# Performance work log

Hardware: AMD Instinct MI355X
Metric: run time of the kernel (lower is better)

## Reference

```python
import jax, jax.numpy as jnp
import numpy as np

DECAY = 0.99
EPS = 1e-05
B, T, DIM, N_EMBED = 64, 1024, 256, 1024


def setup_inputs() -> dict:
    key = jax.random.key(0)
    k1, k2 = jax.random.split(key, 2)
    input_ = jax.random.normal(k1, (B, T, DIM), dtype=jnp.float32)
    embed = jax.random.normal(k2, (DIM, N_EMBED), dtype=jnp.float32)  # buffer 'embed'
    cluster_size = jnp.zeros((N_EMBED,), dtype=jnp.float32)           # buffer 'cluster_size'
    embed_avg = embed.copy()                                          # buffer 'embed_avg'
    return {"input_": input_, "embed": embed, "cluster_size": cluster_size, "embed_avg": embed_avg}


def reference(input_, embed, cluster_size, embed_avg):
    n_embed = embed.shape[1]
    flatten = input_.reshape(-1, embed.shape[0])  # [N, dim]
    dist = (jnp.sum(flatten * flatten, axis=-1, keepdims=True)
            - 2.0 * flatten @ embed
            + jnp.sum(embed * embed, axis=0, keepdims=True))
    embed_ind = jnp.argmin(dist, axis=1)  # (-dist).max(1) == argmin(dist)
    quantize = jnp.take(embed.T, embed_ind, axis=0).reshape(input_.shape)

    # training-mode EMA codebook update (buffers are detached in torch)
    # embed_onehot_sum = onehot.sum(0); embed_sum = flatten.T @ onehot
    # implemented via segment_sum (same math, no NxK one-hot materialized)
    ones = jnp.ones((flatten.shape[0],), dtype=flatten.dtype)
    embed_onehot_sum = jax.ops.segment_sum(ones, embed_ind, num_segments=n_embed)
    embed_sum = jax.ops.segment_sum(flatten, embed_ind, num_segments=n_embed).T  # [dim, n_embed]

    new_cluster_size = cluster_size * DECAY + (1.0 - DECAY) * embed_onehot_sum
    # NOTE: original code applies .mul_(decay) TWICE to embed_avg -> decay**2 (faithful)
    new_embed_avg = embed_avg * (DECAY * DECAY) + (1.0 - DECAY) * embed_sum
    n = jnp.sum(new_cluster_size)
    cs = (new_cluster_size + EPS) / (n + n_embed * EPS) * n
    new_embed = new_embed_avg / cs[None, :]

    diff = jnp.mean((jax.lax.stop_gradient(quantize) - input_) ** 2)
    quantize_st = input_ + jax.lax.stop_gradient(quantize - input_)
    return quantize_st, diff, embed_ind, new_cluster_size, new_embed_avg, new_embed
```

## Files before the change

kernel.cpp:

```cpp
#include <hip/hip_runtime.h>
#include <float.h>

#define DECAY 0.99f
#define EPS 1e-5f
#define NROWS 65536
#define DIM 256
#define NEMB 1024
#define CH 64
#define MAXSUB 2048

#define GLOBAL_AS __attribute__((address_space(1)))
#define LOCAL_AS  __attribute__((address_space(3)))

typedef _Float16 f16;
typedef _Float16 half8 __attribute__((ext_vector_type(8)));
typedef float f32x4 __attribute__((ext_vector_type(4)));

__global__ __launch_bounds__(256) void k_enorm(const float* __restrict__ embed,
                                               float* __restrict__ enorm2,
                                               int* __restrict__ counts) {
    int kk = threadIdx.x & 63;
    int dg = threadIdx.x >> 6;
    int k  = blockIdx.x * 64 + kk;
    float s = 0.f;
    for (int d = dg; d < DIM; d += 4) {
        float v = embed[(size_t)d * NEMB + k];
        s = fmaf(v, v, s);
    }
    __shared__ float red[4][64];
    red[dg][kk] = s;
    __syncthreads();
    if (dg == 0) enorm2[k] = red[0][kk] + red[1][kk] + red[2][kk] + red[3][kk];
    int gt = blockIdx.x * 256 + threadIdx.x;
    if (gt < NEMB) counts[gt] = 0;
}

__global__ __launch_bounds__(256) void k_prep(const float* __restrict__ embed,
                                              float* __restrict__ embedT,
                                              f16* __restrict__ ehlT) {
    __shared__ float tile[32][33];
    int c0 = blockIdx.x * 32, d0 = blockIdx.y * 32;
    int tx = threadIdx.x, ty = threadIdx.y;
#pragma unroll
    for (int i = 0; i < 4; i++)
        tile[ty + 8 * i][tx] = embed[(size_t)(d0 + ty + 8 * i) * NEMB + c0 + tx];
    __syncthreads();
#pragma unroll
    for (int i = 0; i < 4; i++) {
        int c = c0 + ty + 8 * i;
        int d = d0 + tx;
        float v = tile[tx][ty + 8 * i];
        embedT[(size_t)c * DIM + d] = v;
        f16 h = (f16)v;
        ehlT[(size_t)c * 512 + d]       = h;
        ehlT[(size_t)c * 512 + 256 + d] = (f16)(v - (float)h);
    }
}

#define LDS_A  0
#define LDS_B0 131072
#define LDS_B1 147456
#define LDS_SZ 163840

__global__ __launch_bounds__(512, 2) void k_argmin_mfma(const float* __restrict__ input,
                                                        const f16* __restrict__ ehlT,
                                                        const float* __restrict__ enorm2,
                                                        int* __restrict__ ind,
                                                        float* __restrict__ out_ind) {
    __shared__ char lds[LDS_SZ];
    const int tid  = threadIdx.x;
    const int lane = tid & 63;
    const int w    = tid >> 6;
    const int wr   = w >> 2;
    const int wc   = w & 3;
    const int rb   = blockIdx.x * 128;
    const int l15  = lane & 15;
    const int lkh  = lane >> 4;
    const int swa  = (l15 & 7) << 4;
    const int swb  = ((l15 >> 1) & 3) << 4;
    const int slot_log   = (lane & 3) ^ ((lane >> 3) & 3);
    const int gl_laneoff = (lane >> 2) * 512 + slot_log * 8;

#pragma unroll
    for (int i = 0; i < 2; i++) {
        int chunkid = w * 2 + i;
        const f16* src = ehlT + (size_t)chunkid * 8192 + gl_laneoff;
        __builtin_amdgcn_global_load_lds((const GLOBAL_AS unsigned*)src,
            (LOCAL_AS unsigned*)(lds + LDS_B0 + chunkid * 1024), 16, 0, 0);
    }

#pragma unroll
    for (int it8 = 0; it8 < 4; it8++) {
        int task = tid + 512 * it8;
        int row = task >> 4, ch = task & 15;
        const float4* g = (const float4*)(input + (size_t)(rb + row) * DIM + ch * 16);
        float fv[16];
        *(float4*)(fv + 0)  = g[0];
        *(float4*)(fv + 4)  = g[1];
        *(float4*)(fv + 8)  = g[2];
        *(float4*)(fv + 12) = g[3];
        half8 hh[2], llv[2];
#pragma unroll
        for (int u = 0; u < 2; u++)
#pragma unroll
            for (int e = 0; e < 8; e++) {
                float x = fv[u * 8 + e];
                f16 h = (f16)x;
                hh[u][e]  = h;
                llv[u][e] = (f16)(x - (float)h);
            }
        int rbase = row * 1024;
        int sw = (row & 7) << 4;
        *(half8*)(lds + LDS_A + rbase + (((ch * 2    ) * 16) ^ sw)) = hh[0];
        *(half8*)(lds + LDS_A + rbase + (((ch * 2 + 1) * 16) ^ sw)) = hh[1];
        *(half8*)(lds + LDS_A + rbase + (((32 + ch * 2) * 16) ^ sw)) = llv[0];
        *(half8*)(lds + LDS_A + rbase + (((33 + ch * 2) * 16) ^ sw)) = llv[1];
    }
    __syncthreads();

    float bv[16];
    int   bi[16];
#pragma unroll
    for (int q = 0; q < 16; q++) { bv[q] = FLT_MAX; bi[q] = 0x7fffffff; }

    int p = 0;
    for (int ct = 0; ct < 4; ct++) {
        const int cb = ct * 256;
        f32x4 acc[4][4];
#pragma unroll
        for (int fr = 0; fr < 4; fr++)
#pragma unroll
            for (int fc = 0; fc < 4; fc++) acc[fr][fc] = (f32x4){0.f, 0.f, 0.f, 0.f};

        for (int kt = 0; kt < 24; kt++) {
            const int it = ct * 24 + kt;
            if (it < 95) {
                int itn = it + 1;
                int ct2 = itn / 24;
                int kt2 = itn - ct2 * 24;
                int seg2 = kt2 >> 3, kq2 = kt2 & 7;
                int koff2 = ((seg2 == 2) ? 256 : 0) + kq2 * 32;
                const f16* base = ehlT + (size_t)ct2 * 131072 + koff2 + gl_laneoff;
                char* dstb = lds + (p ? LDS_B0 : LDS_B1);
#pragma unroll
                for (int i = 0; i < 2; i++) {
                    int chunkid = w * 2 + i;
                    __builtin_amdgcn_global_load_lds(
                        (const GLOBAL_AS unsigned*)(base + (size_t)chunkid * 8192),
                        (LOCAL_AS unsigned*)(dstb + chunkid * 1024), 16, 0, 0);
                }
            }
            const int seg = kt >> 3, kq = kt & 7;
            const int jslot = ((seg == 1) ? 32 : 0) + kq * 4 + lkh;
            const char* Bb = lds + (p ? LDS_B1 : LDS_B0);
            half8 af[4], bf[4];
#pragma unroll
            for (int f = 0; f < 4; f++) {
                int row = wr * 64 + f * 16 + l15;
                af[f] = *(const half8*)(lds + LDS_A + row * 1024 + ((jslot * 16) ^ swa));
            }
#pragma unroll
            for (int f = 0; f < 4; f++) {
                int col = wc * 64 + f * 16 + l15;
                bf[f] = *(const half8*)(Bb + col * 64 + ((lkh * 16) ^ swb));
            }
#pragma unroll
            for (int fr = 0; fr < 4; fr++)
#pragma unroll
                for (int fc = 0; fc < 4; fc++)
                    acc[fr][fc] = __builtin_amdgcn_mfma_f32_16x16x32_f16(
                        af[fr], bf[fc], acc[fr][fc], 0, 0, 0);
            if (kt == 23) {
#pragma unroll
                for (int fc = 0; fc < 4; fc++) {
                    int col = cb + wc * 64 + fc * 16 + l15;
                    float e2 = enorm2[col];
#pragma unroll
                    for (int fr = 0; fr < 4; fr++)
#pragma unroll
                        for (int r = 0; r < 4; r++) {
                            float s = fmaf(-2.f, acc[fr][fc][r], e2);
                            int q = fr * 4 + r;
                            if (s < bv[q]) { bv[q] = s; bi[q] = col; }
                        }
                }
            }
            __syncthreads();
            p ^= 1;
        }
    }

#pragma unroll
    for (int q = 0; q < 16; q++) {
        float v = bv[q]; int i = bi[q];
#pragma unroll
        for (int m = 1; m <= 8; m <<= 1) {
            float ov = __shfl_xor(v, m, 64);
            int   oi = __shfl_xor(i, m, 64);
            if (ov < v || (ov == v && oi < i)) { v = ov; i = oi; }
        }
        bv[q] = v; bi[q] = i;
    }
    float* PV = (float*)(lds + LDS_B0);
    int*   PI = (int*)(lds + LDS_B0 + 2048);
    if (l15 == 0) {
#pragma unroll
        for (int fr = 0; fr < 4; fr++)
#pragma unroll
            for (int r = 0; r < 4; r++) {
                int rrow = wr * 64 + fr * 16 + lkh * 4 + r;
                PV[rrow * 4 + wc] = bv[fr * 4 + r];
                PI[rrow * 4 + wc] = bi[fr * 4 + r];
            }
    }
    __syncthreads();
    if (tid < 128) {
        float best = FLT_MAX; int bidx = 0x7fffffff;
#pragma unroll
        for (int t = 0; t < 4; t++) {
            float v = PV[tid * 4 + t];
            int   i = PI[tid * 4 + t];
            if (v < best || (v == best && i < bidx)) { best = v; bidx = i; }
        }
        ind[rb + tid] = bidx;
        out_ind[rb + tid] = (float)bidx;
    }
}

__global__ __launch_bounds__(256) void k_quant(const float* __restrict__ input,
                                               const float* __restrict__ embedT,
                                               const int* __restrict__ ind,
                                               float* __restrict__ out_q,
                                               float* __restrict__ partials) {
    const int tid = threadIdx.x;
    const unsigned gid = blockIdx.x * 256 + tid;
    float s = 0.f;
#pragma unroll
    for (int j = 0; j < 8; j++) {
        size_t i4 = (size_t)gid + (size_t)j * 524288u;
        int row = (int)(i4 >> 6);
        int d4  = (int)(i4 & 63);
        float4 iv = *reinterpret_cast<const float4*>(input + i4 * 4);
        int k = ind[row];
        float4 qv = *reinterpret_cast<const float4*>(embedT + (size_t)k * DIM + d4 * 4);
        float dx = qv.x - iv.x, dy = qv.y - iv.y, dz = qv.z - iv.z, dw = qv.w - iv.w;
        float4 ov;
        ov.x = iv.x + dx; ov.y = iv.y + dy; ov.z = iv.z + dz; ov.w = iv.w + dw;
        *reinterpret_cast<float4*>(out_q + i4 * 4) = ov;
        s += dx * dx + dy * dy + dz * dz + dw * dw;
    }
    __shared__ float red[256];
    red[tid] = s;
    __syncthreads();
    for (int off = 128; off > 0; off >>= 1) {
        if (tid < off) red[tid] += red[tid + off];
        __syncthreads();
    }
    if (tid == 0) partials[blockIdx.x] = red[0];
}

__global__ __launch_bounds__(256) void k_diff(const float* __restrict__ partials,
                                              float* __restrict__ out_diff) {
    __shared__ float red[256];
    int tid = threadIdx.x;
    float s = 0.f;
    for (int j = 0; j < 8; j++) s += partials[tid * 8 + j];
    red[tid] = s;
    __syncthreads();
    for (int off = 128; off > 0; off >>= 1) {
        if (tid < off) red[tid] += red[tid + off];
        __syncthreads();
    }
    if (tid == 0) out_diff[0] = red[0] / 16777216.0f;
}

__global__ __launch_bounds__(256) void k_hist(const int* __restrict__ ind,
                                              int* __restrict__ counts) {
    __shared__ int h[NEMB];
    int tid = threadIdx.x;
    for (int j = tid; j < NEMB; j += 256) h[j] = 0;
    __syncthreads();
    for (int i = blockIdx.x * 256 + tid; i < NROWS; i += 64 * 256)
        atomicAdd(&h[ind[i]], 1);
    __syncthreads();
    for (int j = tid; j < NEMB; j += 256)
        if (h[j]) atomicAdd(&counts[j], h[j]);
}

__global__ __launch_bounds__(1024) void k_scan(const int* __restrict__ counts,
                                               const float* __restrict__ cluster_size,
                                               int* __restrict__ offsets,
                                               int* __restrict__ cursor,
                                               int* __restrict__ substart,
                                               float* __restrict__ out_ncs,
                                               float* __restrict__ cs) {
    __shared__ int sh[NEMB];
    __shared__ float shf[NEMB];
    int tid = threadIdx.x;
    int c = counts[tid];
    sh[tid] = c;
    __syncthreads();
    for (int off = 1; off < NEMB; off <<= 1) {
        int t = (tid >= off) ? sh[tid - off] : 0;
        __syncthreads();
        sh[tid] += t;
        __syncthreads();
    }
    int excl = sh[tid] - c;
    offsets[tid] = excl;
    cursor[tid]  = excl;
    int sc = (c + CH - 1) / CH;
    __syncthreads();
    sh[tid] = sc;
    __syncthreads();
    for (int off = 1; off < NEMB; off <<= 1) {
        int t = (tid >= off) ? sh[tid - off] : 0;
        __syncthreads();
        sh[tid] += t;
        __syncthreads();
    }
    substart[tid] = sh[tid] - sc;
    if (tid == NEMB - 1) substart[NEMB] = sh[tid];
    float ncs = cluster_size[tid] * DECAY + (1.f - DECAY) * (float)c;
    out_ncs[tid] = ncs;
    shf[tid] = ncs;
    __syncthreads();
    for (int off = 512; off > 0; off >>= 1) {
        if (tid < off) shf[tid] += shf[tid + off];
        __syncthreads();
    }
    float n = shf[0];
    cs[tid] = (ncs + EPS) / (n + NEMB * EPS) * n;
}

__global__ __launch_bounds__(256) void k_scatter(const int* __restrict__ ind,
                                                 int* __restrict__ cursor,
                                                 int* __restrict__ sorted) {
    int i = blockIdx.x * 256 + threadIdx.x;
    int k = ind[i];
    int pos = atomicAdd(&cursor[k], 1);
    sorted[pos] = i;
}

__global__ __launch_bounds__(256) void k_psum(const float* __restrict__ input,
                                              const int* __restrict__ sorted,
                                              const int* __restrict__ counts,
                                              const int* __restrict__ offsets,
                                              const int* __restrict__ substart,
                                              float* __restrict__ partial) {
    const int b = blockIdx.x;
    if (b >= substart[NEMB]) return;
    int lo = 0, hi = NEMB;
    while (hi - lo > 1) {
        int mid = (lo + hi) >> 1;
        if (substart[mid] <= b) lo = mid; else hi = mid;
    }
    const int k     = lo;
    const int chunk = b - substart[k];
    const int cnt   = counts[k];
    const int base  = offsets[k] + chunk * CH;
    const int lim   = min(CH, cnt - chunk * CH);
    const int d     = threadIdx.x;
    float s = 0.f;
    for (int i = 0; i < lim; i++) {
        int row = sorted[base + i];
        s += input[(size_t)row * DIM + d];
    }
    partial[(size_t)b * DIM + d] = s;
}

__global__ __launch_bounds__(256) void k_ema(const float* __restrict__ partial,
                                             const float* __restrict__ embed_avg,
                                             const int* __restrict__ substart,
                                             const float* __restrict__ cs,
                                             float* __restrict__ out_navg,
                                             float* __restrict__ out_nembed) {
    const int d = blockIdx.x;
    const int t = threadIdx.x;
#pragma unroll
    for (int i = 0; i < 4; i++) {
        int k = t + 256 * i;
        int s0 = substart[k], s1 = substart[k + 1];
        float s = 0.f;
        for (int sub = s0; sub < s1; sub++)
            s += partial[(size_t)sub * DIM + d];
        float navg = embed_avg[(size_t)d * NEMB + k] * (DECAY * DECAY) + (1.f - DECAY) * s;
        out_navg[(size_t)d * NEMB + k] = navg;
        out_nembed[(size_t)d * NEMB + k] = navg / cs[k];
    }
}

extern "C" void kernel_launch(void* const* d_in, const int* in_sizes, int n_in,
                              void* d_out, int out_size, void* d_ws, size_t ws_size,
                              hipStream_t stream) {
    const float* input        = (const float*)d_in[0];
    const float* embed        = (const float*)d_in[1];
    const float* cluster_size = (const float*)d_in[2];
    const float* embed_avg    = (const float*)d_in[3];

    float* out        = (float*)d_out;
    float* out_q      = out;
    float* out_diff   = out + 16777216;
    float* out_ind    = out + 16777217;
    float* out_ncs    = out + 16842753;
    float* out_navg   = out + 16843777;
    float* out_nembed = out + 17105921;

    char* ws = (char*)d_ws;
    size_t o = 0;
    int*   w_ind      = (int*)(ws + o);   o += (size_t)NROWS * 4;
    float* w_embedT   = (float*)(ws + o); o += (size_t)DIM * NEMB * 4;
    float* w_enorm    = (float*)(ws + o); o += NEMB * 4;
    int*   w_counts   = (int*)(ws + o);   o += NEMB * 4;
    int*   w_offsets  = (int*)(ws + o);   o += NEMB * 4;
    int*   w_cursor   = (int*)(ws + o);   o += NEMB * 4;
    float* w_cs       = (float*)(ws + o); o += NEMB * 4;
    float* w_partials = (float*)(ws + o); o += 2048 * 4;
    int*   w_sorted   = (int*)(ws + o);   o += (size_t)NROWS * 4;
    int*   w_substart = (int*)(ws + o);   o += (NEMB + 4) * 4;
    float* w_partial  = (float*)(ws + o); o += (size_t)MAXSUB * DIM * 4;
    f16*   w_ehlT     = (f16*)(ws + o);   o += (size_t)NEMB * 512 * 2;

    k_enorm<<<16, 256, 0, stream>>>(embed, w_enorm, w_counts);
    k_prep<<<dim3(32, 8), dim3(32, 8), 0, stream>>>(embed, w_embedT, w_ehlT);
    k_argmin_mfma<<<NROWS / 128, 512, 0, stream>>>(input, w_ehlT, w_enorm, w_ind, out_ind);
    k_quant<<<2048, 256, 0, stream>>>(input, w_embedT, w_ind, out_q, w_partials);
    k_diff<<<1, 256, 0, stream>>>(w_partials, out_diff);
    k_hist<<<64, 256, 0, stream>>>(w_ind, w_counts);
    k_scan<<<1, 1024, 0, stream>>>(w_counts, cluster_size, w_offsets, w_cursor,
                                   w_substart, out_ncs, w_cs);
    k_scatter<<<NROWS / 256, 256, 0, stream>>>(w_ind, w_cursor, w_sorted);
    k_psum<<<MAXSUB, 256, 0, stream>>>(input, w_sorted, w_counts, w_offsets,
                                       w_substart, w_partial);
    k_ema<<<DIM, 256, 0, stream>>>(w_partial, embed_avg, w_substart, w_cs,
                                   out_navg, out_nembed);
}
```

Measured before the change: 294.2 us.

## Pre-split input to fp16 hi/lo and restructure argmin GEMM with 256-row tiles

Adds a separate kernel that splits the fp32 input into fp16 high/low parts and stores them in the quantize output buffer as scratch. The argmin kernel now processes 256 rows per block, streaming both A and B tiles through double-buffered LDS with direct global-to-LDS loads and explicit vmcnt waits. It also keeps per-slab partial minima in LDS instead of registers and raises MFMA priority. The aim is more reuse per B tile and better overlap of loads with MFMA, at the cost of an extra pass over the input, more accumulator registers, and only 256 blocks.

Measured after the change: 343.0 us. +16.6%, slower.

```diff
diff --git a/kernel.cpp b/kernel.cpp
--- a/kernel.cpp
+++ b/kernel.cpp
@@ -57,169 +57,180 @@
     }
 }
 
-#define LDS_A  0
-#define LDS_B0 131072
-#define LDS_B1 147456
-#define LDS_SZ 163840
-
-__global__ __launch_bounds__(512, 2) void k_argmin_mfma(const float* __restrict__ input,
+__global__ __launch_bounds__(512) void k_xsplit(const float* __restrict__ input,
+                                                f16* __restrict__ xhl) {
+    int g = blockIdx.x * 512 + threadIdx.x;
+    int row = g >> 5, dq = g & 31;
+    const float4* s = (const float4*)(input + (size_t)row * DIM + dq * 8);
+    float4 v0 = s[0], v1 = s[1];
+    float fv[8] = {v0.x, v0.y, v0.z, v0.w, v1.x, v1.y, v1.z, v1.w};
+    half8 h, l;
+#pragma unroll
+    for (int e = 0; e < 8; ++e) {
+        f16 hh = (f16)fv[e];
+        h[e] = hh;
+        l[e] = (f16)(fv[e] - (float)hh);
+    }
+    *(half8*)(xhl + (size_t)row * 512 + dq * 8)       = h;
+    *(half8*)(xhl + (size_t)row * 512 + 256 + dq * 8) = l;
+}
+
+#define LDS_A0 0
+#define LDS_A1 32768
+#define LDS_B0 65536
+#define LDS_B1 98304
+#define LDS_PV 131072
+#define LDS_PI 135168
+#define LDS_SZ 139264
+
+__device__ __forceinline__ void stage_tile(const f16* __restrict__ xhl,
+                                           const f16* __restrict__ ehlT,
+                                           char* dA, char* dB,
+                                           int rb, int gn, int w, int rA, int ksx) {
+    int slab_n = gn / 12, kt_n = gn % 12;
+    int ka = (kt_n < 4) ? kt_n * 64 : (kt_n < 8 ? 256 + (kt_n - 4) * 64 : (kt_n - 8) * 64);
+    int kb = (kt_n < 4) ? kt_n * 64 : (kt_n < 8 ? (kt_n - 4) * 64 : 256 + (kt_n - 8) * 64);
+    int cbn = slab_n * 256;
+#pragma unroll
+    for (int j = 0; j < 4; ++j) {
+        const f16* s = xhl + (size_t)(rb + j * 64 + w * 8 + rA) * 512 + ka + ksx * 8;
+        __builtin_amdgcn_global_load_lds((const GLOBAL_AS unsigned*)s,
+            (LOCAL_AS unsigned*)(dA + (j * 8 + w) * 1024), 16, 0, 0);
+    }
+#pragma unroll
+    for (int j = 0; j < 4; ++j) {
+        const f16* s = ehlT + (size_t)(cbn + j * 64 + w * 8 + rA) * 512 + kb + ksx * 8;
+        __builtin_amdgcn_global_load_lds((const GLOBAL_AS unsigned*)s,
+            (LOCAL_AS unsigned*)(dB + (j * 8 + w) * 1024), 16, 0, 0);
+    }
+}
+
+__global__ __launch_bounds__(512, 2) void k_argmin_mfma(const f16* __restrict__ xhl,
                                                         const f16* __restrict__ ehlT,
                                                         const float* __restrict__ enorm2,
                                                         int* __restrict__ ind,
                                                         float* __restrict__ out_ind) {
     __shared__ char lds[LDS_SZ];
+    float* PV = (float*)(lds + LDS_PV);
+    int*   PI = (int*)(lds + LDS_PI);
     const int tid  = threadIdx.x;
     const int lane = tid & 63;
     const int w    = tid >> 6;
     const int wr   = w >> 2;
     const int wc   = w & 3;
-    const int rb   = blockIdx.x * 128;
+    const int rb   = blockIdx.x * 256;
     const int l15  = lane & 15;
     const int lkh  = lane >> 4;
-    const int swa  = (l15 & 7) << 4;
-    const int swb  = ((l15 >> 1) & 3) << 4;
-    const int slot_log   = (lane & 3) ^ ((lane >> 3) & 3);
-    const int gl_laneoff = (lane >> 2) * 512 + slot_log * 8;
-
-#pragma unroll
-    for (int i = 0; i < 2; i++) {
-        int chunkid = w * 2 + i;
-        const f16* src = ehlT + (size_t)chunkid * 8192 + gl_laneoff;
-        __builtin_amdgcn_global_load_lds((const GLOBAL_AS unsigned*)src,
-            (LOCAL_AS unsigned*)(lds + LDS_B0 + chunkid * 1024), 16, 0, 0);
-    }
-
-#pragma unroll
-    for (int it8 = 0; it8 < 4; it8++) {
-        int task = tid + 512 * it8;
-        int row = task >> 4, ch = task & 15;
-        const float4* g = (const float4*)(input + (size_t)(rb + row) * DIM + ch * 16);
-        float fv[16];
-        *(float4*)(fv + 0)  = g[0];
-        *(float4*)(fv + 4)  = g[1];
-        *(float4*)(fv + 8)  = g[2];
-        *(float4*)(fv + 12) = g[3];
-        half8 hh[2], llv[2];
-#pragma unroll
-        for (int u = 0; u < 2; u++)
-#pragma unroll
-            for (int e = 0; e < 8; e++) {
-                float x = fv[u * 8 + e];
-                f16 h = (f16)x;
-                hh[u][e]  = h;
-                llv[u][e] = (f16)(x - (float)h);
-            }
-        int rbase = row * 1024;
-        int sw = (row & 7) << 4;
-        *(half8*)(lds + LDS_A + rbase + (((ch * 2    ) * 16) ^ sw)) = hh[0];
-        *(half8*)(lds + LDS_A + rbase + (((ch * 2 + 1) * 16) ^ sw)) = hh[1];
-        *(half8*)(lds + LDS_A + rbase + (((32 + ch * 2) * 16) ^ sw)) = llv[0];
-        *(half8*)(lds + LDS_A + rbase + (((33 + ch * 2) * 16) ^ sw)) = llv[1];
-    }
-    __syncthreads();
-
-    float bv[16];
-    int   bi[16];
-#pragma unroll
-    for (int q = 0; q < 16; q++) { bv[q] = FLT_MAX; bi[q] = 0x7fffffff; }
+    const int rA   = lane >> 3;
+    const int ksx  = (lane & 7) ^ (lane >> 3);
+
+    PV[tid] = FLT_MAX; PV[tid + 512] = FLT_MAX;
+    PI[tid] = 0x7fffffff; PI[tid + 512] = 0x7fffffff;
+
+    float e2a[4][4];
+#pragma unroll
+    for (int s = 0; s < 4; ++s)
+#pragma unroll
+        for (int fc = 0; fc < 4; ++fc)
+            e2a[s][fc] = enorm2[s * 256 + wc * 64 + fc * 16 + l15];
+
+    f32x4 acc[8][4];
+#pragma unroll
+    for (int i = 0; i < 8; ++i)
+#pragma unroll
+        for (int j = 0; j < 4; ++j) acc[i][j] = (f32x4){0.f, 0.f, 0.f, 0.f};
+
+    stage_tile(xhl, ehlT, lds + LDS_A0, lds + LDS_B0, rb, 0, w, rA, ksx);
 
     int p = 0;
-    for (int ct = 0; ct < 4; ct++) {
-        const int cb = ct * 256;
-        f32x4 acc[4][4];
-#pragma unroll
-        for (int fr = 0; fr < 4; fr++)
-#pragma unroll
-            for (int fc = 0; fc < 4; fc++) acc[fr][fc] = (f32x4){0.f, 0.f, 0.f, 0.f};
-
-        for (int kt = 0; kt < 24; kt++) {
-            const int it = ct * 24 + kt;
-            if (it < 95) {
-                int itn = it + 1;
-                int ct2 = itn / 24;
-                int kt2 = itn - ct2 * 24;
-                int seg2 = kt2 >> 3, kq2 = kt2 & 7;
-                int koff2 = ((seg2 == 2) ? 256 : 0) + kq2 * 32;
-                const f16* base = ehlT + (size_t)ct2 * 131072 + koff2 + gl_laneoff;
-                char* dstb = lds + (p ? LDS_B0 : LDS_B1);
-#pragma unroll
-                for (int i = 0; i < 2; i++) {
-                    int chunkid = w * 2 + i;
-                    __builtin_amdgcn_global_load_lds(
-                        (const GLOBAL_AS unsigned*)(base + (size_t)chunkid * 8192),
-                        (LOCAL_AS unsigned*)(dstb + chunkid * 1024), 16, 0, 0);
+    for (int g = 0; g < 48; ++g) {
+        asm volatile("" ::: "memory");
+        __builtin_amdgcn_s_barrier();
+        asm volatile("" ::: "memory");
+        if (g < 47) {
+            stage_tile(xhl, ehlT,
+                       lds + (p ? LDS_A0 : LDS_A1), lds + (p ? LDS_B0 : LDS_B1),
+                       rb, g + 1, w, rA, ksx);
+            asm volatile("s_waitcnt vmcnt(8)" ::: "memory");
+        } else {
+            asm volatile("s_waitcnt vmcnt(0)" ::: "memory");
+        }
+        __builtin_amdgcn_s_barrier();
+        __builtin_amdgcn_sched_barrier(0);
+
+        const char* A = lds + (p ? LDS_A1 : LDS_A0);
+        const char* B = lds + (p ? LDS_B1 : LDS_B0);
+        half8 bf[4];
+#pragma unroll
+        for (int q = 0; q < 4; ++q) {
+            const int ks = q >> 1, h = q & 1;
+            if (h == 0) {
+#pragma unroll
+                for (int fc = 0; fc < 4; ++fc) {
+                    int col = wc * 64 + fc * 16 + l15;
+                    bf[fc] = *(const half8*)(B + col * 128 +
+                                             (((ks * 4 + lkh) * 16) ^ ((col & 7) << 4)));
                 }
             }
-            const int seg = kt >> 3, kq = kt & 7;
-            const int jslot = ((seg == 1) ? 32 : 0) + kq * 4 + lkh;
-            const char* Bb = lds + (p ? LDS_B1 : LDS_B0);
-            half8 af[4], bf[4];
-#pragma unroll
-            for (int f = 0; f < 4; f++) {
-                int row = wr * 64 + f * 16 + l15;
-                af[f] = *(const half8*)(lds + LDS_A + row * 1024 + ((jslot * 16) ^ swa));
+            half8 af[4];
+#pragma unroll
+            for (int f = 0; f < 4; ++f) {
+                int row = wr * 128 + (h * 4 + f) * 16 + l15;
+                af[f] = *(const half8*)(A + row * 128 +
+                                        (((ks * 4 + lkh) * 16) ^ ((row & 7) << 4)));
             }
-#pragma unroll
-            for (int f = 0; f < 4; f++) {
-                int col = wc * 64 + f * 16 + l15;
-                bf[f] = *(const half8*)(Bb + col * 64 + ((lkh * 16) ^ swb));
-            }
-#pragma unroll
-            for (int fr = 0; fr < 4; fr++)
-#pragma unroll
-                for (int fc = 0; fc < 4; fc++)
-                    acc[fr][fc] = __builtin_amdgcn_mfma_f32_16x16x32_f16(
-                        af[fr], bf[fc], acc[fr][fc], 0, 0, 0);
-            if (kt == 23) {
-#pragma unroll
-                for (int fc = 0; fc < 4; fc++) {
-                    int col = cb + wc * 64 + fc * 16 + l15;
-                    float e2 = enorm2[col];
-#pragma unroll
-                    for (int fr = 0; fr < 4; fr++)
-#pragma unroll
-                        for (int r = 0; r < 4; r++) {
-                            float s = fmaf(-2.f, acc[fr][fc][r], e2);
-                            int q = fr * 4 + r;
-                            if (s < bv[q]) { bv[q] = s; bi[q] = col; }
+            __builtin_amdgcn_s_setprio(1);
+#pragma unroll
+            for (int f = 0; f < 4; ++f)
+#pragma unroll
+                for (int fc = 0; fc < 4; ++fc)
+                    acc[h * 4 + f][fc] = __builtin_amdgcn_mfma_f32_16x16x32_f16(
+                        af[f], bf[fc], acc[h * 4 + f][fc], 0, 0, 0);
+            __builtin_amdgcn_s_setprio(0);
+        }
+
+        if ((g % 12) == 11) {
+            const int slab = g / 12;
+            const int cb = slab * 256;
+#pragma unroll
+            for (int fr = 0; fr < 8; ++fr)
+#pragma unroll
+                for (int r = 0; r < 4; ++r) {
+                    float best = FLT_MAX; int bidx = 0x7fffffff;
+#pragma unroll
+                    for (int fc = 0; fc < 4; ++fc) {
+                        float sc = fmaf(-2.f, acc[fr][fc][r], e2a[slab][fc]);
+                        int col = cb + wc * 64 + fc * 16 + l15;
+                        if (sc < best) { best = sc; bidx = col; }
+                    }
+#pragma unroll
+                    for (int m = 1; m <= 8; m <<= 1) {
+                        float ov = __shfl_xor(best, m, 64);
+                        int   oi = __shfl_xor(bidx, m, 64);
+                        if (ov < best || (ov == best && oi < bidx)) { best = ov; bidx = oi; }
+                    }
+                    if (l15 == 0) {
+                        int row = wr * 128 + fr * 16 + lkh * 4 + r;
+                        float pv = PV[row * 4 + wc]; int pi = PI[row * 4 + wc];
+                        if (best < pv || (best == pv && bidx < pi)) {
+                            PV[row * 4 + wc] = best; PI[row * 4 + wc] = bidx;
                         }
+                    }
                 }
-            }
-            __syncthreads();
-            p ^= 1;
+#pragma unroll
+            for (int i = 0; i < 8; ++i)
+#pragma unroll
+                for (int j = 0; j < 4; ++j) acc[i][j] = (f32x4){0.f, 0.f, 0.f, 0.f};
         }
-    }
-
-#pragma unroll
-    for (int q = 0; q < 16; q++) {
-        float v = bv[q]; int i = bi[q];
-#pragma unroll
-        for (int m = 1; m <= 8; m <<= 1) {
-            float ov = __shfl_xor(v, m, 64);
-            int   oi = __shfl_xor(i, m, 64);
-            if (ov < v || (ov == v && oi < i)) { v = ov; i = oi; }
-        }
-        bv[q] = v; bi[q] = i;
-    }
-    float* PV = (float*)(lds + LDS_B0);
-    int*   PI = (int*)(lds + LDS_B0 + 2048);
-    if (l15 == 0) {
-#pragma unroll
-        for (int fr = 0; fr < 4; fr++)
-#pragma unroll
-            for (int r = 0; r < 4; r++) {
-                int rrow = wr * 64 + fr * 16 + lkh * 4 + r;
-                PV[rrow * 4 + wc] = bv[fr * 4 + r];
-                PI[rrow * 4 + wc] = bi[fr * 4 + r];
-            }
-    }
-    __syncthreads();
-    if (tid < 128) {
-        float best = FLT_MAX; int bidx = 0x7fffffff;
-#pragma unroll
-        for (int t = 0; t < 4; t++) {
-            float v = PV[tid * 4 + t];
-            int   i = PI[tid * 4 + t];
+        p ^= 1;
+    }
+
+    __syncthreads();
+    if (tid < 256) {
+        float best = PV[tid * 4]; int bidx = PI[tid * 4];
+#pragma unroll
+        for (int t = 1; t < 4; ++t) {
+            float v = PV[tid * 4 + t]; int i = PI[tid * 4 + t];
             if (v < best || (v == best && i < bidx)) { best = v; bidx = i; }
         }
         ind[rb + tid] = bidx;
@@ -405,6 +416,8 @@
     float* out_ncs    = out + 16842753;
     float* out_navg   = out + 16843777;
     float* out_nembed = out + 17105921;
+
+    f16* xhl = (f16*)out_q;
 
     char* ws = (char*)d_ws;
     size_t o = 0;
@@ -423,7 +436,8 @@
 
     k_enorm<<<16, 256, 0, stream>>>(embed, w_enorm, w_counts);
     k_prep<<<dim3(32, 8), dim3(32, 8), 0, stream>>>(embed, w_embedT, w_ehlT);
-    k_argmin_mfma<<<NROWS / 128, 512, 0, stream>>>(input, w_ehlT, w_enorm, w_ind, out_ind);
+    k_xsplit<<<4096, 512, 0, stream>>>(input, xhl);
+    k_argmin_mfma<<<256, 512, 0, stream>>>(xhl, w_ehlT, w_enorm, w_ind, out_ind);
     k_quant<<<2048, 256, 0, stream>>>(input, w_embedT, w_ind, out_q, w_partials);
     k_diff<<<1, 256, 0, stream>>>(w_partials, out_diff);
     k_hist<<<64, 256, 0, stream>>>(w_ind, w_counts);
```

## Load codebook fragments directly from global, fuse histogram and diff reduction

Applied to the files above, without the earlier changes.

The argmin kernel drops the double-buffered global_load_lds staging of codebook tiles and the per-iteration __syncthreads, and reads B fragments straight from global/L2 into registers with the k-loop fully unrolled. The histogram is folded into the argmin kernel as one global atomicAdd per row, and the diff reduction is merged into the scan kernel, which removes two launches. This trades LDS traffic and barriers for uncoalesced global reads of B per wave, and adds global atomic contention on counts. It also shrinks LDS use.

Result: slower. 647.7 us (+120.2%).

```diff
diff --git a/kernel.cpp b/kernel.cpp
--- a/kernel.cpp
+++ b/kernel.cpp
@@ -8,9 +8,6 @@
 #define NEMB 1024
 #define CH 64
 #define MAXSUB 2048
-
-#define GLOBAL_AS __attribute__((address_space(1)))
-#define LOCAL_AS  __attribute__((address_space(3)))
 
 typedef _Float16 f16;
 typedef _Float16 half8 __attribute__((ext_vector_type(8)));
@@ -58,15 +55,16 @@
 }
 
 #define LDS_A  0
-#define LDS_B0 131072
-#define LDS_B1 147456
-#define LDS_SZ 163840
+#define LDS_PV 131072
+#define LDS_PI 133120
+#define LDS_SZ 135168
 
 __global__ __launch_bounds__(512, 2) void k_argmin_mfma(const float* __restrict__ input,
                                                         const f16* __restrict__ ehlT,
                                                         const float* __restrict__ enorm2,
                                                         int* __restrict__ ind,
-                                                        float* __restrict__ out_ind) {
+                                                        float* __restrict__ out_ind,
+                                                        int* __restrict__ counts) {
     __shared__ char lds[LDS_SZ];
     const int tid  = threadIdx.x;
     const int lane = tid & 63;
@@ -77,17 +75,6 @@
     const int l15  = lane & 15;
     const int lkh  = lane >> 4;
     const int swa  = (l15 & 7) << 4;
-    const int swb  = ((l15 >> 1) & 3) << 4;
-    const int slot_log   = (lane & 3) ^ ((lane >> 3) & 3);
-    const int gl_laneoff = (lane >> 2) * 512 + slot_log * 8;
-
-#pragma unroll
-    for (int i = 0; i < 2; i++) {
-        int chunkid = w * 2 + i;
-        const f16* src = ehlT + (size_t)chunkid * 8192 + gl_laneoff;
-        __builtin_amdgcn_global_load_lds((const GLOBAL_AS unsigned*)src,
-            (LOCAL_AS unsigned*)(lds + LDS_B0 + chunkid * 1024), 16, 0, 0);
-    }
 
 #pragma unroll
     for (int it8 = 0; it8 < 4; it8++) {
@@ -123,46 +110,35 @@
 #pragma unroll
     for (int q = 0; q < 16; q++) { bv[q] = FLT_MAX; bi[q] = 0x7fffffff; }
 
-    int p = 0;
     for (int ct = 0; ct < 4; ct++) {
         const int cb = ct * 256;
+        const f16* bp0 = ehlT + (size_t)(cb + wc * 64 +  0 + l15) * 512 + lkh * 8;
+        const f16* bp1 = ehlT + (size_t)(cb + wc * 64 + 16 + l15) * 512 + lkh * 8;
+        const f16* bp2 = ehlT + (size_t)(cb + wc * 64 + 32 + l15) * 512 + lkh * 8;
+        const f16* bp3 = ehlT + (size_t)(cb + wc * 64 + 48 + l15) * 512 + lkh * 8;
+
         f32x4 acc[4][4];
 #pragma unroll
         for (int fr = 0; fr < 4; fr++)
 #pragma unroll
             for (int fc = 0; fc < 4; fc++) acc[fr][fc] = (f32x4){0.f, 0.f, 0.f, 0.f};
 
+#pragma unroll
         for (int kt = 0; kt < 24; kt++) {
-            const int it = ct * 24 + kt;
-            if (it < 95) {
-                int itn = it + 1;
-                int ct2 = itn / 24;
-                int kt2 = itn - ct2 * 24;
-                int seg2 = kt2 >> 3, kq2 = kt2 & 7;
-                int koff2 = ((seg2 == 2) ? 256 : 0) + kq2 * 32;
-                const f16* base = ehlT + (size_t)ct2 * 131072 + koff2 + gl_laneoff;
-                char* dstb = lds + (p ? LDS_B0 : LDS_B1);
-#pragma unroll
-                for (int i = 0; i < 2; i++) {
-                    int chunkid = w * 2 + i;
-                    __builtin_amdgcn_global_load_lds(
-                        (const GLOBAL_AS unsigned*)(base + (size_t)chunkid * 8192),
-                        (LOCAL_AS unsigned*)(dstb + chunkid * 1024), 16, 0, 0);
-                }
-            }
             const int seg = kt >> 3, kq = kt & 7;
+            const int boff = ((seg == 2) ? 256 : 0) + kq * 32;
+            half8 bf[4];
+            bf[0] = *(const half8*)(bp0 + boff);
+            bf[1] = *(const half8*)(bp1 + boff);
+            bf[2] = *(const half8*)(bp2 + boff);
+            bf[3] = *(const half8*)(bp3 + boff);
             const int jslot = ((seg == 1) ? 32 : 0) + kq * 4 + lkh;
-            const char* Bb = lds + (p ? LDS_B1 : LDS_B0);
-            half8 af[4], bf[4];
+            const int koff = (jslot * 16) ^ swa;
+            half8 af[4];
 #pragma unroll
             for (int f = 0; f < 4; f++) {
                 int row = wr * 64 + f * 16 + l15;
-                af[f] = *(const half8*)(lds + LDS_A + row * 1024 + ((jslot * 16) ^ swa));
-            }
-#pragma unroll
-            for (int f = 0; f < 4; f++) {
-                int col = wc * 64 + f * 16 + l15;
-                bf[f] = *(const half8*)(Bb + col * 64 + ((lkh * 16) ^ swb));
+                af[f] = *(const half8*)(lds + LDS_A + row * 1024 + koff);
             }
 #pragma unroll
             for (int fr = 0; fr < 4; fr++)
@@ -170,23 +146,20 @@
                 for (int fc = 0; fc < 4; fc++)
                     acc[fr][fc] = __builtin_amdgcn_mfma_f32_16x16x32_f16(
                         af[fr], bf[fc], acc[fr][fc], 0, 0, 0);
-            if (kt == 23) {
-#pragma unroll
-                for (int fc = 0; fc < 4; fc++) {
-                    int col = cb + wc * 64 + fc * 16 + l15;
-                    float e2 = enorm2[col];
-#pragma unroll
-                    for (int fr = 0; fr < 4; fr++)
-#pragma unroll
-                        for (int r = 0; r < 4; r++) {
-                            float s = fmaf(-2.f, acc[fr][fc][r], e2);
-                            int q = fr * 4 + r;
-                            if (s < bv[q]) { bv[q] = s; bi[q] = col; }
-                        }
+        }
+
+#pragma unroll
+        for (int fc = 0; fc < 4; fc++) {
+            int col = cb + wc * 64 + fc * 16 + l15;
+            float e2 = enorm2[col];
+#pragma unroll
+            for (int fr = 0; fr < 4; fr++)
+#pragma unroll
+                for (int r = 0; r < 4; r++) {
+                    float s = fmaf(-2.f, acc[fr][fc][r], e2);
+                    int q = fr * 4 + r;
+                    if (s < bv[q]) { bv[q] = s; bi[q] = col; }
                 }
-            }
-            __syncthreads();
-            p ^= 1;
         }
     }
 
@@ -201,8 +174,8 @@
         }
         bv[q] = v; bi[q] = i;
     }
-    float* PV = (float*)(lds + LDS_B0);
-    int*   PI = (int*)(lds + LDS_B0 + 2048);
+    float* PV = (float*)(lds + LDS_PV);
+    int*   PI = (int*)(lds + LDS_PI);
     if (l15 == 0) {
 #pragma unroll
         for (int fr = 0; fr < 4; fr++)
@@ -224,6 +197,7 @@
         }
         ind[rb + tid] = bidx;
         out_ind[rb + tid] = (float)bidx;
+        atomicAdd(&counts[bidx], 1);
     }
 }
 
@@ -259,44 +233,26 @@
     if (tid == 0) partials[blockIdx.x] = red[0];
 }
 
-__global__ __launch_bounds__(256) void k_diff(const float* __restrict__ partials,
-                                              float* __restrict__ out_diff) {
-    __shared__ float red[256];
-    int tid = threadIdx.x;
-    float s = 0.f;
-    for (int j = 0; j < 8; j++) s += partials[tid * 8 + j];
-    red[tid] = s;
-    __syncthreads();
-    for (int off = 128; off > 0; off >>= 1) {
-        if (tid < off) red[tid] += red[tid + off];
-        __syncthreads();
-    }
-    if (tid == 0) out_diff[0] = red[0] / 16777216.0f;
-}
-
-__global__ __launch_bounds__(256) void k_hist(const int* __restrict__ ind,
-                                              int* __restrict__ counts) {
-    __shared__ int h[NEMB];
-    int tid = threadIdx.x;
-    for (int j = tid; j < NEMB; j += 256) h[j] = 0;
-    __syncthreads();
-    for (int i = blockIdx.x * 256 + tid; i < NROWS; i += 64 * 256)
-        atomicAdd(&h[ind[i]], 1);
-    __syncthreads();
-    for (int j = tid; j < NEMB; j += 256)
-        if (h[j]) atomicAdd(&counts[j], h[j]);
-}
-
 __global__ __launch_bounds__(1024) void k_scan(const int* __restrict__ counts,
                                                const float* __restrict__ cluster_size,
+                                               const float* __restrict__ qpartials,
                                                int* __restrict__ offsets,
                                                int* __restrict__ cursor,
                                                int* __restrict__ substart,
                                                float* __restrict__ out_ncs,
-                                               float* __restrict__ cs) {
+                                               float* __restrict__ cs,
+                                               float* __restrict__ out_diff) {
     __shared__ int sh[NEMB];
     __shared__ float shf[NEMB];
     int tid = threadIdx.x;
+    shf[tid] = qpartials[tid] + qpartials[tid + 1024];
+    __syncthreads();
+    for (int off = 512; off > 0; off >>= 1) {
+        if (tid < off) shf[tid] += shf[tid + off];
+        __syncthreads();
+    }
+    if (tid == 0) out_diff[0] = shf[0] / 16777216.0f;
+    __syncthreads();
     int c = counts[tid];
     sh[tid] = c;
     __syncthreads();
@@ -423,12 +379,11 @@
 
     k_enorm<<<16, 256, 0, stream>>>(embed, w_enorm, w_counts);
     k_prep<<<dim3(32, 8), dim3(32, 8), 0, stream>>>(embed, w_embedT, w_ehlT);
-    k_argmin_mfma<<<NROWS / 128, 512, 0, stream>>>(input, w_ehlT, w_enorm, w_ind, out_ind);
+    k_argmin_mfma<<<NROWS / 128, 512, 0, stream>>>(input, w_ehlT, w_enorm,
+                                                   w_ind, out_ind, w_counts);
     k_quant<<<2048, 256, 0, stream>>>(input, w_embedT, w_ind, out_q, w_partials);
-    k_diff<<<1, 256, 0, stream>>>(w_partials, out_diff);
-    k_hist<<<64, 256, 0, stream>>>(w_ind, w_counts);
-    k_scan<<<1, 1024, 0, stream>>>(w_counts, cluster_size, w_offsets, w_cursor,
-                                   w_substart, out_ncs, w_cs);
+    k_scan<<<1, 1024, 0, stream>>>(w_counts, cluster_size, w_partials, w_offsets,
+                                   w_cursor, w_substart, out_ncs, w_cs, out_diff);
     k_scatter<<<NROWS / 256, 256, 0, stream>>>(w_ind, w_cursor, w_sorted);
     k_psum<<<MAXSUB, 256, 0, stream>>>(input, w_sorted, w_counts, w_offsets,
                                        w_substart, w_partial);
```

## Fuse histogram and diff reduction; tighten argmin pipeline with manual waitcnt barriers

Applied to the files above, without the earlier changes.

Removes the separate histogram and diff-reduction kernels: counts are accumulated with global atomics at the end of the argmin kernel, and the loss partials are reduced inside the scan kernel. In the MFMA loop, the full __syncthreads is replaced by explicit vmcnt waits plus raw s_barrier, and MFMA issue priority is raised with setprio. Codebook norms are preloaded into registers. This cuts two launches and some synchronization overhead, at the cost of more register pressure and up to 65536 global atomics into 1024 counters.

Result: slower. 309.3 us (+5.1%).

```diff
diff --git a/kernel.cpp b/kernel.cpp
--- a/kernel.cpp
+++ b/kernel.cpp
@@ -66,7 +66,8 @@
                                                         const f16* __restrict__ ehlT,
                                                         const float* __restrict__ enorm2,
                                                         int* __restrict__ ind,
-                                                        float* __restrict__ out_ind) {
+                                                        float* __restrict__ out_ind,
+                                                        int* __restrict__ counts) {
     __shared__ char lds[LDS_SZ];
     const int tid  = threadIdx.x;
     const int lane = tid & 63;
@@ -81,6 +82,13 @@
     const int slot_log   = (lane & 3) ^ ((lane >> 3) & 3);
     const int gl_laneoff = (lane >> 2) * 512 + slot_log * 8;
 
+    float e2a[4][4];
+#pragma unroll
+    for (int s = 0; s < 4; ++s)
+#pragma unroll
+        for (int fc = 0; fc < 4; ++fc)
+            e2a[s][fc] = enorm2[s * 256 + wc * 64 + fc * 16 + l15];
+
 #pragma unroll
     for (int i = 0; i < 2; i++) {
         int chunkid = w * 2 + i;
@@ -149,7 +157,13 @@
                         (const GLOBAL_AS unsigned*)(base + (size_t)chunkid * 8192),
                         (LOCAL_AS unsigned*)(dstb + chunkid * 1024), 16, 0, 0);
                 }
-            }
+                asm volatile("s_waitcnt vmcnt(2)" ::: "memory");
+            } else {
+                asm volatile("s_waitcnt vmcnt(0)" ::: "memory");
+            }
+            __builtin_amdgcn_s_barrier();
+            __builtin_amdgcn_sched_barrier(0);
+
             const int seg = kt >> 3, kq = kt & 7;
             const int jslot = ((seg == 1) ? 32 : 0) + kq * 4 + lkh;
             const char* Bb = lds + (p ? LDS_B1 : LDS_B0);
@@ -164,17 +178,20 @@
                 int col = wc * 64 + f * 16 + l15;
                 bf[f] = *(const half8*)(Bb + col * 64 + ((lkh * 16) ^ swb));
             }
+            __builtin_amdgcn_s_setprio(1);
 #pragma unroll
             for (int fr = 0; fr < 4; fr++)
 #pragma unroll
                 for (int fc = 0; fc < 4; fc++)
                     acc[fr][fc] = __builtin_amdgcn_mfma_f32_16x16x32_f16(
                         af[fr], bf[fc], acc[fr][fc], 0, 0, 0);
+            __builtin_amdgcn_s_setprio(0);
+
             if (kt == 23) {
 #pragma unroll
                 for (int fc = 0; fc < 4; fc++) {
                     int col = cb + wc * 64 + fc * 16 + l15;
-                    float e2 = enorm2[col];
+                    float e2 = e2a[ct][fc];
 #pragma unroll
                     for (int fr = 0; fr < 4; fr++)
 #pragma unroll
@@ -185,7 +202,7 @@
                         }
                 }
             }
-            __syncthreads();
+            __builtin_amdgcn_s_barrier();
             p ^= 1;
         }
     }
@@ -224,6 +241,7 @@
         }
         ind[rb + tid] = bidx;
         out_ind[rb + tid] = (float)bidx;
+        atomicAdd(&counts[bidx], 1);
     }
 }
 
@@ -259,44 +277,26 @@
     if (tid == 0) partials[blockIdx.x] = red[0];
 }
 
-__global__ __launch_bounds__(256) void k_diff(const float* __restrict__ partials,
-                                              float* __restrict__ out_diff) {
-    __shared__ float red[256];
-    int tid = threadIdx.x;
-    float s = 0.f;
-    for (int j = 0; j < 8; j++) s += partials[tid * 8 + j];
-    red[tid] = s;
-    __syncthreads();
-    for (int off = 128; off > 0; off >>= 1) {
-        if (tid < off) red[tid] += red[tid + off];
-        __syncthreads();
-    }
-    if (tid == 0) out_diff[0] = red[0] / 16777216.0f;
-}
-
-__global__ __launch_bounds__(256) void k_hist(const int* __restrict__ ind,
-                                              int* __restrict__ counts) {
-    __shared__ int h[NEMB];
-    int tid = threadIdx.x;
-    for (int j = tid; j < NEMB; j += 256) h[j] = 0;
-    __syncthreads();
-    for (int i = blockIdx.x * 256 + tid; i < NROWS; i += 64 * 256)
-        atomicAdd(&h[ind[i]], 1);
-    __syncthreads();
-    for (int j = tid; j < NEMB; j += 256)
-        if (h[j]) atomicAdd(&counts[j], h[j]);
-}
-
 __global__ __launch_bounds__(1024) void k_scan(const int* __restrict__ counts,
                                                const float* __restrict__ cluster_size,
+                                               const float* __restrict__ qpartials,
                                                int* __restrict__ offsets,
                                                int* __restrict__ cursor,
                                                int* __restrict__ substart,
                                                float* __restrict__ out_ncs,
-                                               float* __restrict__ cs) {
+                                               float* __restrict__ cs,
+                                               float* __restrict__ out_diff) {
     __shared__ int sh[NEMB];
     __shared__ float shf[NEMB];
     int tid = threadIdx.x;
+    shf[tid] = qpartials[tid] + qpartials[tid + 1024];
+    __syncthreads();
+    for (int off = 512; off > 0; off >>= 1) {
+        if (tid < off) shf[tid] += shf[tid + off];
+        __syncthreads();
+    }
+    if (tid == 0) out_diff[0] = shf[0] / 16777216.0f;
+    __syncthreads();
     int c = counts[tid];
     sh[tid] = c;
     __syncthreads();
@@ -423,12 +423,11 @@
 
     k_enorm<<<16, 256, 0, stream>>>(embed, w_enorm, w_counts);
     k_prep<<<dim3(32, 8), dim3(32, 8), 0, stream>>>(embed, w_embedT, w_ehlT);
-    k_argmin_mfma<<<NROWS / 128, 512, 0, stream>>>(input, w_ehlT, w_enorm, w_ind, out_ind);
+    k_argmin_mfma<<<NROWS / 128, 512, 0, stream>>>(input, w_ehlT, w_enorm,
+                                                   w_ind, out_ind, w_counts);
     k_quant<<<2048, 256, 0, stream>>>(input, w_embedT, w_ind, out_q, w_partials);
-    k_diff<<<1, 256, 0, stream>>>(w_partials, out_diff);
-    k_hist<<<64, 256, 0, stream>>>(w_ind, w_counts);
-    k_scan<<<1, 1024, 0, stream>>>(w_counts, cluster_size, w_offsets, w_cursor,
-                                   w_substart, out_ncs, w_cs);
+    k_scan<<<1, 1024, 0, stream>>>(w_counts, cluster_size, w_partials, w_offsets,
+                                   w_cursor, w_substart, out_ncs, w_cs, out_diff);
     k_scatter<<<NROWS / 256, 256, 0, stream>>>(w_ind, w_cursor, w_sorted);
     k_psum<<<MAXSUB, 256, 0, stream>>>(input, w_sorted, w_counts, w_offsets,
                                        w_substart, w_partial);
```
